# Optimization experiments

Hardware: AMD Instinct MI355X
Metric: run time of the kernel (lower is better)

## Reference

```python
import jax, jax.numpy as jnp
import numpy as np


def _bilinear_gather(corr, x, y):
    # corr: [N, H2, W2]; x, y: [N, K, K] pixel coords; zero padding outside,
    # matching F.grid_sample(mode='bilinear', padding_mode='zeros', align_corners=True).
    N, H2, W2 = corr.shape
    corr_flat = corr.reshape(N, H2 * W2)
    x0 = jnp.floor(x)
    y0 = jnp.floor(y)
    wx1 = x - x0
    wy1 = y - y0

    def gather(xi, yi):
        valid = (xi >= 0) & (xi <= W2 - 1) & (yi >= 0) & (yi <= H2 - 1)
        xc = jnp.clip(xi, 0, W2 - 1).astype(jnp.int32)
        yc = jnp.clip(yi, 0, H2 - 1).astype(jnp.int32)
        idx = (yc * W2 + xc).reshape(N, -1)
        vals = jnp.take_along_axis(corr_flat, idx, axis=1).reshape(xi.shape)
        return jnp.where(valid, vals, jnp.zeros((), corr.dtype))

    return (gather(x0, y0) * (1 - wx1) * (1 - wy1)
            + gather(x0 + 1, y0) * wx1 * (1 - wy1)
            + gather(x0, y0 + 1) * (1 - wx1) * wy1
            + gather(x0 + 1, y0 + 1) * wx1 * wy1)


def setup_inputs() -> dict:
    key = jax.random.key(0)
    k1, k2, k3 = jax.random.split(key, 3)
    B, D, H, W = 2, 256, 64, 64
    fmap1 = jax.random.normal(k1, (B, D, H, W), dtype=jnp.float32)
    fmap2 = jax.random.normal(k2, (B, D, H, W), dtype=jnp.float32)
    # coords in pixel space [0, W-1]
    coords = jax.random.uniform(k3, (B, 2, H, W), dtype=jnp.float32) * (W - 1)
    return {"fmap1": fmap1, "fmap2": fmap2, "coords": coords, "radius": 4}


def reference(fmap1, fmap2, coords, radius):
    B, D, H, W = fmap1.shape
    # all-pairs correlation: [B, H*W, H*W], scaled by 1/sqrt(D)
    f1 = fmap1.reshape(B, D, H * W)
    f2 = fmap2.reshape(B, D, H * W)
    corr = jnp.einsum('bdn,bdm->bnm', f1, f2) / jnp.sqrt(jnp.asarray(D, jnp.float32))
    corr = corr.reshape(B * H * W, H, W)

    r = radius
    K = 2 * r + 1
    d = jnp.linspace(-r, r, K, dtype=jnp.float32)
    dyg, dxg = jnp.meshgrid(d, d, indexing='ij')
    delta = jnp.stack([dyg, dxg], axis=-1)  # [K, K, 2] (matches torch.meshgrid(dy, dx))

    centroid = coords.transpose(0, 2, 3, 1).reshape(B * H * W, 1, 1, 2)
    coords_lvl = centroid + delta[None]  # [N, K, K, 2]
    # RAFT bilinear_sampler: channel 0 is x, channel 1 is y
    x = coords_lvl[..., 0]
    y = coords_lvl[..., 1]

    out = _bilinear_gather(corr, x, y)  # [N, K, K]
    out = out.reshape(B, H, W, K * K).transpose(0, 3, 1, 2)
    return out.astype(jnp.float32)
```

## Files before the change

### kernel.cpp

```cpp
#include <hip/hip_runtime.h>

#define HWC 4096
#define WC 64
#define HC 64
#define DC 256
#define BC 2
#define KKC 81

typedef _Float16 h2 __attribute__((ext_vector_type(2)));
typedef _Float16 h8 __attribute__((ext_vector_type(8)));

static __device__ inline float dot8(h8 v, h8 a, float s) {
#if __has_builtin(__builtin_amdgcn_fdot2)
    s = __builtin_amdgcn_fdot2((h2){v[0], v[1]}, (h2){a[0], a[1]}, s, false);
    s = __builtin_amdgcn_fdot2((h2){v[2], v[3]}, (h2){a[2], a[3]}, s, false);
    s = __builtin_amdgcn_fdot2((h2){v[4], v[5]}, (h2){a[4], a[5]}, s, false);
    s = __builtin_amdgcn_fdot2((h2){v[6], v[7]}, (h2){a[6], a[7]}, s, false);
#else
#pragma unroll
    for (int k = 0; k < 8; ++k) s += (float)v[k] * (float)a[k];
#endif
    return s;
}

#define DPP_ADD(x, ctrl) \
    ((x) + __int_as_float(__builtin_amdgcn_update_dpp(0, __float_as_int(x), (ctrl), 0xF, 0xF, true)))

__global__ __launch_bounds__(256) void transpose_h_k(const float* __restrict__ f1,
                                                     const float* __restrict__ f2,
                                                     _Float16* __restrict__ o1,
                                                     _Float16* __restrict__ o2) {
    __shared__ float tile[64][33];
    const int z = blockIdx.z;
    const int b = z & 1;
    const float* in = (z >> 1) ? f2 : f1;
    _Float16* out = (z >> 1) ? o2 : o1;
    in += (size_t)b * DC * HWC;
    out += (size_t)b * HWC * DC;

    const int m0 = blockIdx.x * 32, d0 = blockIdx.y * 64;
    const int tid = threadIdx.x;
    const int tx = tid & 31, ty = tid >> 5;
#pragma unroll
    for (int k = 0; k < 8; ++k)
        tile[ty + k * 8][tx] = in[(size_t)(d0 + ty + k * 8) * HWC + m0 + tx];
    __syncthreads();

    const int dx = tid & 7, my = tid >> 3;
    h8 v;
#pragma unroll
    for (int e = 0; e < 8; ++e) v[e] = (_Float16)tile[dx * 8 + e][my];
    *(h8*)(out + (size_t)(m0 + my) * DC + d0 + dx * 8) = v;
}

__global__ __launch_bounds__(256) void corr_k(const _Float16* __restrict__ f1t,
                                              const _Float16* __restrict__ f2t,
                                              const float* __restrict__ coords,
                                              float* __restrict__ out) {
    __shared__ float Cs[112];

    const int bid = blockIdx.x;
    const int xcd = bid & 7;
    const int b = xcd >> 2;
    const int hw = ((bid >> 3) << 2) + (xcd & 3);

    const int tid = threadIdx.x;
    const int g = tid >> 4;
    const int l = tid & 15;

    const float x = coords[((size_t)b * 2 + 0) * HWC + hw];
    const float y = coords[((size_t)b * 2 + 1) * HWC + hw];
    const float x0f = floorf(x), y0f = floorf(y);
    const float wx = x - x0f, wy = y - y0f;
    const int ix0 = (int)x0f, iy0 = (int)y0f;

    const h8* ap = (const h8*)f1t + ((size_t)(b * HWC + hw)) * 32 + l * 2;
    const h8 a0 = ap[0], a1 = ap[1];
    const h8* f2b = (const h8*)f2t + (size_t)b * HWC * 32;

    h8 v0[7], v1[7];
    float vm[7];
#pragma unroll
    for (int it = 0; it < 7; ++it) {
        int t = it * 16 + g;
        t = t > 99 ? 99 : t;
        const int yi = t / 10, xi = t - yi * 10;
        const int gy = iy0 - 4 + yi, gx = ix0 - 4 + xi;
        const bool valid = ((unsigned)gy < (unsigned)HC) & ((unsigned)gx < (unsigned)WC);
        const int gyc = min(max(gy, 0), HC - 1);
        const int gxc = min(max(gx, 0), WC - 1);
        const h8* vp = f2b + (size_t)(gyc * WC + gxc) * 32 + l * 2;
        v0[it] = vp[0];
        v1[it] = vp[1];
        vm[it] = valid ? 0.0625f : 0.f;
    }

#pragma unroll
    for (int it = 0; it < 7; ++it) {
        float s = dot8(v0[it], a0, 0.f);
        s = dot8(v1[it], a1, s);
        s *= vm[it];
        s = DPP_ADD(s, 0xB1);
        s = DPP_ADD(s, 0x4E);
        s = DPP_ADD(s, 0x124);
        s = DPP_ADD(s, 0x128);
        const int t = it * 16 + g;
        if (l == 0 && t < 100) Cs[t] = s;
    }
    __syncthreads();

    if (tid < KKC) {
        const int i = tid / 9, j = tid % 9;
        const float w00 = (1.f - wx) * (1.f - wy);
        const float w01 = wx * (1.f - wy);
        const float w10 = (1.f - wx) * wy;
        const float w11 = wx * wy;
        const float r = w00 * Cs[j * 10 + i]       + w01 * Cs[j * 10 + i + 1] +
                        w10 * Cs[(j + 1) * 10 + i] + w11 * Cs[(j + 1) * 10 + i + 1];
        out[((size_t)(b * KKC + tid)) * HWC + hw] = r;
    }
}

extern "C" void kernel_launch(void* const* d_in, const int* in_sizes, int n_in,
                              void* d_out, int out_size, void* d_ws, size_t ws_size,
                              hipStream_t stream) {
    const float* fmap1 = (const float*)d_in[0];
    const float* fmap2 = (const float*)d_in[1];
    const float* coords = (const float*)d_in[2];
    float* out = (float*)d_out;

    const size_t perH = (size_t)BC * HWC * DC;
    _Float16* f1t = (_Float16*)d_ws;
    _Float16* f2t = f1t + perH;

    transpose_h_k<<<dim3(HWC / 32, DC / 64, 4), dim3(256), 0, stream>>>(fmap1, fmap2, f1t, f2t);
    corr_k<<<dim3(BC * HWC), dim3(256), 0, stream>>>(f1t, f2t, coords, out);
}
```

Baseline: 92.51 us.

## Bucket-sort query pixels by y-coordinate to improve L2 locality of gathers

Adds a small counting-sort kernel that orders each batch's query pixels by floor(y), then corr_k maps blocks to pixels in that sorted order. Blocks running at the same time on an XCD then gather overlapping rows of fmap2, which should raise L2 hit rates for the 10x10 neighborhood loads. In exchange it adds a kernel launch and an extra indirection read, and the output writes become scattered instead of coalesced across blocks.

Measured after the change: 97.34 us. 1.05x slower.

```diff
diff --git a/kernel.cpp b/kernel.cpp
--- a/kernel.cpp
+++ b/kernel.cpp
@@ -53,16 +53,49 @@
     *(h8*)(out + (size_t)(m0 + my) * DC + d0 + dx * 8) = v;
 }
 
+__global__ __launch_bounds__(1024) void sort_k(const float* __restrict__ coords,
+                                               int* __restrict__ sorted) {
+    __shared__ int hist[64];
+    __shared__ int base[64];
+    const int b = blockIdx.x;
+    const int tid = threadIdx.x;
+    if (tid < 64) hist[tid] = 0;
+    __syncthreads();
+    int key[4];
+#pragma unroll
+    for (int k = 0; k < 4; ++k) {
+        const int hw = tid * 4 + k;
+        const float y = coords[((size_t)b * 2 + 1) * HWC + hw];
+        key[k] = min(max((int)floorf(y), 0), 63);
+        atomicAdd(&hist[key[k]], 1);
+    }
+    __syncthreads();
+    if (tid == 0) {
+        int acc = 0;
+        for (int i = 0; i < 64; ++i) { base[i] = acc; acc += hist[i]; }
+    }
+    __syncthreads();
+#pragma unroll
+    for (int k = 0; k < 4; ++k) {
+        const int hw = tid * 4 + k;
+        const int pos = atomicAdd(&base[key[k]], 1);
+        sorted[b * HWC + pos] = hw;
+    }
+}
+
 __global__ __launch_bounds__(256) void corr_k(const _Float16* __restrict__ f1t,
                                               const _Float16* __restrict__ f2t,
                                               const float* __restrict__ coords,
+                                              const int* __restrict__ sorted,
                                               float* __restrict__ out) {
     __shared__ float Cs[112];
 
     const int bid = blockIdx.x;
-    const int xcd = bid & 7;
-    const int b = xcd >> 2;
-    const int hw = ((bid >> 3) << 2) + (xcd & 3);
+    const int x8 = bid & 7;
+    const int b = x8 >> 2;
+    const int q = x8 & 3;
+    const int s = bid >> 3;
+    const int hw = sorted[b * HWC + q * 1024 + s];
 
     const int tid = threadIdx.x;
     const int g = tid >> 4;
@@ -97,15 +130,15 @@
 
 #pragma unroll
     for (int it = 0; it < 7; ++it) {
-        float s = dot8(v0[it], a0, 0.f);
-        s = dot8(v1[it], a1, s);
-        s *= vm[it];
-        s = DPP_ADD(s, 0xB1);
-        s = DPP_ADD(s, 0x4E);
-        s = DPP_ADD(s, 0x124);
-        s = DPP_ADD(s, 0x128);
+        float s2 = dot8(v0[it], a0, 0.f);
+        s2 = dot8(v1[it], a1, s2);
+        s2 *= vm[it];
+        s2 = DPP_ADD(s2, 0xB1);
+        s2 = DPP_ADD(s2, 0x4E);
+        s2 = DPP_ADD(s2, 0x124);
+        s2 = DPP_ADD(s2, 0x128);
         const int t = it * 16 + g;
-        if (l == 0 && t < 100) Cs[t] = s;
+        if (l == 0 && t < 100) Cs[t] = s2;
     }
     __syncthreads();
 
@@ -132,7 +165,9 @@
     const size_t perH = (size_t)BC * HWC * DC;
     _Float16* f1t = (_Float16*)d_ws;
     _Float16* f2t = f1t + perH;
+    int* sorted = (int*)(f2t + perH);
 
     transpose_h_k<<<dim3(HWC / 32, DC / 64, 4), dim3(256), 0, stream>>>(fmap1, fmap2, f1t, f2t);
-    corr_k<<<dim3(BC * HWC), dim3(256), 0, stream>>>(f1t, f2t, coords, out);
+    sort_k<<<dim3(BC), dim3(1024), 0, stream>>>(coords, sorted);
+    corr_k<<<dim3(BC * HWC), dim3(256), 0, stream>>>(f1t, f2t, coords, sorted, out);
 }
```
